# Optimization experiments

Measured on AMD Instinct MI355X. Metric: run time of the kernel, lower is better.

Reference implementation:

```python
import jax, jax.numpy as jnp
import numpy as np
from jax import lax

N = 16384      # total nodes (NG graphs x PER nodes)
PER = 512      # nodes per graph
NG = 32        # number of graphs
E = 262144     # edges (avg degree 16)
NEG = jnp.float32(-1e30)


def gcn_conv(x, W, b, src, dst, em, n):
    # PyG GCNConv: h = xW; add *remaining* self-loops; symmetric norm; aggregate at dst; + bias
    h = x @ W
    w = em.astype(x.dtype)
    selfw = jax.ops.segment_sum(jnp.where((src == dst) & em, 1.0, 0.0), dst, num_segments=n)
    has_self = (selfw > 0).astype(x.dtype)
    deg = jax.ops.segment_sum(w, dst, num_segments=n) + (1.0 - has_self)
    dinv = lax.rsqrt(deg)
    norm = dinv[src] * dinv[dst] * w                      # [E]
    agg = jax.ops.segment_sum(norm[:, None] * h[src], dst, num_segments=n)
    return agg + ((1.0 - has_self) / deg)[:, None] * h + b


def edge_pool(x, src, dst, em, nvalid, Pw, Pb, n):
    # PyG EdgePooling with softmax edge scores, add_to_edge_score=0.1, eval-mode dropout (identity)
    e = src.shape[0]
    raw = (jnp.concatenate([x[src], x[dst]], axis=1) @ Pw)[:, 0] + Pb[0]
    # softmax over edges grouped by target node
    logits = jnp.where(em, raw, NEG)
    mx = jax.ops.segment_max(logits, dst, num_segments=n)
    ex = jnp.where(em, jnp.exp(raw - mx[dst]), 0.0)
    den = jax.ops.segment_sum(ex, dst, num_segments=n)
    score = jnp.where(em, ex / jnp.maximum(den[dst], 1e-16), 0.0) + 0.1
    # greedy sequential edge contraction in descending score order (matches PyG __merge_edges__)
    key = lax.stop_gradient(jnp.where(em, score, NEG))
    order = jnp.argsort(-key)

    def step(marked, sdm):
        s, d, mk = sdm
        ok = mk & ~marked[s] & ~marked[d]
        m1 = marked.at[s].set(marked[s] | ok)
        m2 = m1.at[d].set(m1[d] | ok)
        return m2, ok

    _, ch_sorted = lax.scan(step, ~nvalid, (src[order], dst[order], em[order]))
    chosen = jnp.zeros(e, bool).at[order].set(ch_sorted)

    rep = jnp.minimum(src, dst)
    oth = jnp.maximum(src, dst)
    SEN = n  # out-of-range index -> dropped scatter
    cluster = jnp.arange(n, dtype=src.dtype).at[jnp.where(chosen, oth, SEN)].set(rep, mode='drop')
    node_score = jnp.ones(n, x.dtype).at[jnp.where(chosen, rep, SEN)].set(score, mode='drop')
    absorbed = jnp.zeros(n, bool).at[jnp.where(chosen & (src != dst), oth, SEN)].set(True, mode='drop')
    new_valid = nvalid & ~absorbed
    # new_x[c] = (sum of x over cluster) * edge score (1 for unmatched nodes)
    new_x = jax.ops.segment_sum(x, cluster, num_segments=n) * node_score[:, None]
    new_x = new_x * new_valid[:, None].astype(x.dtype)
    # remap + coalesce edges (dedupe); padding kept via mask
    ns, nd = cluster[src], cluster[dst]
    ekey = jnp.where(em, ns * n + nd, n * n)
    eo = jnp.argsort(ekey)
    ks = ekey[eo]
    dup = jnp.concatenate([jnp.zeros(1, bool), ks[1:] == ks[:-1]])
    return new_x, ns[eo], nd[eo], (ks < n * n) & ~dup, new_valid


def _forward(x, W1, b1, W2, b2, W3, b3, P1w, P1b, P2w, P2b, P3w, P3b,
             L1w, L1b, L2w, L2b, L3w, L3b, edge_index, batch):
    n = x.shape[0]
    src, dst = edge_index[0], edge_index[1]
    em = jnp.ones(src.shape[0], bool)
    nv = jnp.ones(n, bool)
    h = gcn_conv(x, W1, b1, src, dst, em, n)
    h, src, dst, em, nv = edge_pool(h, src, dst, em, nv, P1w, P1b, n)
    h = jax.nn.relu(h)
    h = gcn_conv(h, W2, b2, src, dst, em, n)
    h, src, dst, em, nv = edge_pool(h, src, dst, em, nv, P2w, P2b, n)
    h = jax.nn.relu(h)
    h = gcn_conv(h, W3, b3, src, dst, em, n)
    h, src, dst, em, nv = edge_pool(h, src, dst, em, nv, P3w, P3b, n)
    h = jax.nn.relu(h)
    beff = jnp.where(nv, batch, NG)                       # invalid nodes -> dummy segment
    g = jax.ops.segment_max(h, beff, num_segments=NG + 1)[:NG]
    z = jax.nn.relu(g @ L1w + L1b)
    z = jax.nn.relu(z @ L2w + L2b)
    z = jax.nn.relu(z @ L3w + L3b)
    return jax.nn.softmax(z, axis=-1)


def _lin(k, fi, fo):
    w = jax.random.normal(k, (fi, fo), jnp.float32) * (1.0 / np.sqrt(fi))
    return w, jnp.zeros((fo,), jnp.float32)


def setup_inputs() -> dict:
    key = jax.random.key(0)
    ks = jax.random.split(key, 16)
    x = jax.random.normal(ks[0], (N, 107), jnp.float32)
    src = jax.random.randint(ks[1], (E,), 0, N, dtype=jnp.int32)
    dst = (src // PER) * PER + jax.random.randint(ks[2], (E,), 0, PER, dtype=jnp.int32)
    edge_index = jnp.stack([src, dst])
    batch = jnp.arange(N, dtype=jnp.int32) // PER
    W1, b1 = _lin(ks[3], 107, 200)
    W2, b2 = _lin(ks[4], 200, 400)
    W3, b3 = _lin(ks[5], 400, 600)
    P1w, P1b = _lin(ks[6], 400, 1)
    P2w, P2b = _lin(ks[7], 800, 1)
    P3w, P3b = _lin(ks[8], 1200, 1)
    L1w, L1b = _lin(ks[9], 600, 200)
    L2w, L2b = _lin(ks[10], 200, 20)
    L3w, L3b = _lin(ks[11], 20, 4)
    return dict(x=x, edge_index=edge_index, batch=batch,
                W1=W1, b1=b1, W2=W2, b2=b2, W3=W3, b3=b3,
                P1w=P1w, P1b=P1b, P2w=P2w, P2b=P2b, P3w=P3w, P3b=P3b,
                L1w=L1w, L1b=L1b, L2w=L2w, L2b=L2b, L3w=L3w, L3b=L3b)


def reference(x, edge_index, batch, W1, b1, W2, b2, W3, b3,
              P1w, P1b, P2w, P2b, P3w, P3b, L1w, L1b, L2w, L2b, L3w, L3b):
    return _forward(x, W1, b1, W2, b2, W3, b3, P1w, P1b, P2w, P2b, P3w, P3b,
                    L1w, L1b, L2w, L2b, L3w, L3b, edge_index, batch)
```

## Files before the change

### kernel.cpp

```cpp
#include <hip/hip_runtime.h>

#define NN 16384
#define PERG 512
#define NGR 32
#define NE 262144
#define GSEG 9216

__device__ __forceinline__ unsigned encf(float f){
  unsigned u = __float_as_uint(f);
  return (u & 0x80000000u) ? ~u : (u | 0x80000000u);
}
__device__ __forceinline__ float decf(unsigned e){
  unsigned u = (e & 0x80000000u) ? (e ^ 0x80000000u) : ~e;
  return __uint_as_float(u);
}

__global__ void k_padx(const float* __restrict__ x, float* __restrict__ xp){
  int i = blockIdx.x*256 + threadIdx.x;
  if (i < NN*112){ int r = i/112, c = i-r*112; xp[i] = (c<107) ? x[r*107+c] : 0.f; }
}
__global__ void k_padw(const float* __restrict__ Wsrc, float* __restrict__ Wdst,
                       int Ksrc, int Kdst, int N){
  int i = blockIdx.x*256 + threadIdx.x;
  if (i < Kdst*N){ int r = i/N, c = i-r*N; Wdst[i] = (r<Ksrc) ? Wsrc[r*N+c] : 0.f; }
}

__global__ __launch_bounds__(256) void k_bucket(const int* __restrict__ ei, int* __restrict__ gcount,
    int* __restrict__ bsrc, int* __restrict__ bdst, int* __restrict__ bem, int* __restrict__ beid){
  __shared__ int cnt[NGR];
  __shared__ int base[NGR];
  int t = threadIdx.x;
  if (t < NGR) cnt[t] = 0;
  __syncthreads();
  int e = blockIdx.x*256 + t;
  int s=0,d=0,g=0,r=0;
  bool ok = (e < NE);
  if (ok){ s = ei[e]; d = ei[NE+e]; g = s >> 9; r = atomicAdd(&cnt[g],1); }
  __syncthreads();
  if (t < NGR) base[t] = atomicAdd(&gcount[t], cnt[t]);
  __syncthreads();
  if (ok){
    int pos = g*GSEG + base[g] + r;
    bsrc[pos]=s; bdst[pos]=d; bem[pos]=1; beid[pos]=e;
  }
}
__global__ void k_init_nodes(int* __restrict__ valid){
  int i = blockIdx.x*256 + threadIdx.x;
  if (i < NN) valid[i]=1;
}

__global__ __launch_bounds__(256) void k_mm(const float* __restrict__ A, const float* __restrict__ W,
                                            float* __restrict__ C, int KP, int N){
  __shared__ float As[16][132];
  __shared__ float Ws[16][132];
  int col0 = blockIdx.x*128, row0 = blockIdx.y*128;
  int t = threadIdx.x;
  int tx = t & 15, ty = t >> 4;
  int ar  = t >> 1;
  int akq0 = (t&1)*2, akq1 = (t&1)*2 + 1;
  int wk0 = (2*t) >> 5, wn0 = (2*t) & 31;
  int wk1 = (2*t+1) >> 5, wn1 = (2*t+1) & 31;
  int wc0 = col0 + wn0*4, wc1 = col0 + wn1*4;

  float4 a0,a1,w0,w1;
  auto loadT = [&](int k0){
    a0 = *(const float4*)&A[(size_t)(row0+ar)*KP + k0 + akq0*4];
    a1 = *(const float4*)&A[(size_t)(row0+ar)*KP + k0 + akq1*4];
    const float* p0 = &W[(size_t)(k0+wk0)*N + wc0];
    const float* p1 = &W[(size_t)(k0+wk1)*N + wc1];
    if (wc0+3 < N) w0 = *(const float4*)p0;
    else { w0.x=(wc0<N)?p0[0]:0.f; w0.y=(wc0+1<N)?p0[1]:0.f; w0.z=(wc0+2<N)?p0[2]:0.f; w0.w=0.f; }
    if (wc1+3 < N) w1 = *(const float4*)p1;
    else { w1.x=(wc1<N)?p1[0]:0.f; w1.y=(wc1+1<N)?p1[1]:0.f; w1.z=(wc1+2<N)?p1[2]:0.f; w1.w=0.f; }
  };
  auto storeT = [&](){
    As[akq0*4+0][ar]=a0.x; As[akq0*4+1][ar]=a0.y; As[akq0*4+2][ar]=a0.z; As[akq0*4+3][ar]=a0.w;
    As[akq1*4+0][ar]=a1.x; As[akq1*4+1][ar]=a1.y; As[akq1*4+2][ar]=a1.z; As[akq1*4+3][ar]=a1.w;
    *(float4*)&Ws[wk0][wn0*4] = w0;
    *(float4*)&Ws[wk1][wn1*4] = w1;
  };

  float acc[8][8];
#pragma unroll
  for (int i=0;i<8;i++)
#pragma unroll
    for (int j=0;j<8;j++) acc[i][j]=0.f;

  auto compute = [&](){
#pragma unroll
    for (int kk=0;kk<16;kk++){
      float4 A0 = *(const float4*)&As[kk][ty*4];
      float4 A1 = *(const float4*)&As[kk][64+ty*4];
      float4 B0 = *(const float4*)&Ws[kk][tx*4];
      float4 B1 = *(const float4*)&Ws[kk][64+tx*4];
      float a[8] = {A0.x,A0.y,A0.z,A0.w,A1.x,A1.y,A1.z,A1.w};
      float b[8] = {B0.x,B0.y,B0.z,B0.w,B1.x,B1.y,B1.z,B1.w};
#pragma unroll
      for (int i=0;i<8;i++)
#pragma unroll
        for (int j=0;j<8;j++) acc[i][j] += a[i]*b[j];
    }
  };

  loadT(0);
  storeT();
  __syncthreads();
  for (int k0=16; k0<KP; k0+=16){
    loadT(k0);
    compute();
    __syncthreads();
    storeT();
    __syncthreads();
  }
  compute();

#pragma unroll
  for (int i=0;i<8;i++){
    int r = row0 + ((i<4)? ty*4+i : 64+ty*4+(i-4));
#pragma unroll
    for (int j=0;j<8;j++){
      int cc = col0 + ((j<4)? tx*4+j : 64+tx*4+(j-4));
      if (cc<N) C[(size_t)r*N+cc] = acc[i][j];
    }
  }
}

__global__ __launch_bounds__(1024) void k_prep(const int* __restrict__ bsrc, const int* __restrict__ bdst,
    const int* __restrict__ bem, const int* __restrict__ gcount,
    int* __restrict__ row_s, int* __restrict__ row_e, int* __restrict__ elist,
    float* __restrict__ dinv, float* __restrict__ selfco){
  int g = blockIdx.x, t = threadIdx.x;
  __shared__ int cnt_l[PERG];
  __shared__ int scn[PERG];
  __shared__ int cur[PERG];
  __shared__ unsigned char hs_l[PERG];
  if (t<PERG){ cnt_l[t]=0; hs_l[t]=0; }
  __syncthreads();
  int nE = min(gcount[g], GSEG); int base = g*GSEG;
  for (int k=t;k<nE;k+=1024){
    if (bem[base+k]){
      int d = bdst[base+k]&511;
      atomicAdd(&cnt_l[d],1);
      if (bsrc[base+k]==bdst[base+k]) hs_l[d]=1;
    }
  }
  __syncthreads();
  if (t<PERG) scn[t]=cnt_l[t];
  __syncthreads();
  for (int off=1; off<PERG; off<<=1){
    int v = (t<PERG && t>=off) ? scn[t-off] : 0;
    __syncthreads();
    if (t<PERG) scn[t]+=v;
    __syncthreads();
  }
  if (t<PERG){
    int excl = scn[t]-cnt_l[t];
    row_s[g*PERG+t] = base+excl;
    row_e[g*PERG+t] = base+scn[t];
    cur[t] = excl;
    float deg = (float)cnt_l[t] + (hs_l[t]?0.f:1.f);
    dinv[g*PERG+t]   = rsqrtf(deg);
    selfco[g*PERG+t] = hs_l[t]?0.f:(1.f/deg);
  }
  __syncthreads();
  for (int k=t;k<nE;k+=1024){
    if (bem[base+k]){
      int d = bdst[base+k]&511;
      elist[base + atomicAdd(&cur[d],1)] = base+k;
    }
  }
}

template<int FO>
__global__ __launch_bounds__(256) void k_aggab(const float* __restrict__ h, const int* __restrict__ row_s,
    const int* __restrict__ row_e, const int* __restrict__ elist, const int* __restrict__ bsrc,
    const float* __restrict__ dinv, const float* __restrict__ selfco, const float* __restrict__ bias,
    const float* __restrict__ Pw, float* __restrict__ y, float* __restrict__ aval, float* __restrict__ bval){
  constexpr int Q = (FO+63)/64;
  int lane = threadIdx.x & 63;
  int nblk = (blockIdx.x & 7)*512 + (blockIdx.x >> 3);
  int i = nblk*4 + (threadIdx.x>>6);
  float acc[Q];
#pragma unroll
  for (int q=0;q<Q;q++) acc[q]=0.f;
  int s0 = row_s[i], s1 = row_e[i];
  float di = dinv[i];
  for (int p=s0; p<s1; p++){
    int e = elist[p]; int s = bsrc[e];
    float nr = di * dinv[s];
    const float* hrow = h + (size_t)s*FO;
#pragma unroll
    for (int q=0;q<Q;q++){ int c=lane+q*64; if (c<FO) acc[q] += nr*hrow[c]; }
  }
  float sc = selfco[i];
  const float* hi = h + (size_t)i*FO;
  float* yi = y + (size_t)i*FO;
  float sa=0.f, sb=0.f;
#pragma unroll
  for (int q=0;q<Q;q++){
    int c = lane+q*64;
    if (c<FO){
      float v = acc[q] + sc*hi[c] + bias[c];
      yi[c] = v;
      sa += v*Pw[c];
      sb += v*Pw[FO+c];
    }
  }
  for (int o=32;o;o>>=1){ sa += __shfl_xor(sa,o); sb += __shfl_xor(sb,o); }
  if (lane==0){ aval[i]=sa; bval[i]=sb; }
}

#define NEPT 9
__global__ __launch_bounds__(1024) void k_pool(const int* __restrict__ gcount,
    int* __restrict__ bsrc, int* __restrict__ bdst, int* __restrict__ bem, const int* __restrict__ beid,
    const float* __restrict__ aval, const float* __restrict__ bval, const float* __restrict__ Pb,
    float* __restrict__ nscore, int* __restrict__ partner, int* __restrict__ valid, int* __restrict__ table){
  int g = blockIdx.x, t = threadIdx.x;
  __shared__ unsigned mx[PERG];
  __shared__ float den[PERG];
  __shared__ unsigned long long best[PERG];
  __shared__ unsigned char marked[PERG];
  __shared__ unsigned short clus[PERG];
  __shared__ int flag;
  int nE = min(gcount[g], GSEG), base = g*GSEG;
  if (t<PERG){
    mx[t]=0u; den[t]=0.f;
    marked[t] = valid[g*PERG+t] ? 0 : 1;
    clus[t] = (unsigned short)t;
    nscore[g*PERG+t] = 1.f;
    partner[g*PERG+t] = -1;
  }
  __syncthreads();

  int sL[NEPT], dL[NEPT];
  float rawv[NEPT];
  unsigned em = 0u;
#pragma unroll
  for (int j=0;j<NEPT;j++){
    sL[j]=0; dL[j]=0; rawv[j]=0.f;
    int k = t + j*1024;
    if (k < nE && bem[base+k]){
      sL[j] = bsrc[base+k]&511; dL[j] = bdst[base+k]&511;
      rawv[j] = aval[(g<<9)+sL[j]] + bval[(g<<9)+dL[j]] + Pb[0];
      em |= (1u<<j);
      atomicMax(&mx[dL[j]], encf(rawv[j]));
    }
  }
  __syncthreads();
  float exv[NEPT];
#pragma unroll
  for (int j=0;j<NEPT;j++){
    exv[j]=0.f;
    if (em & (1u<<j)){
      exv[j] = expf(rawv[j] - decf(mx[dL[j]]));
      atomicAdd(&den[dL[j]], exv[j]);
    }
  }
  __syncthreads();
  unsigned long long pri[NEPT];
#pragma unroll
  for (int j=0;j<NEPT;j++){
    pri[j]=0ull;
    if (em & (1u<<j)){
      int k = t + j*1024;
      float sc = exv[j]/fmaxf(den[dL[j]],1e-16f) + 0.1f;
      pri[j] = ((unsigned long long)__float_as_uint(sc) << 18)
             | (unsigned long long)(0x3FFFFu - (unsigned)beid[base+k]);
    }
  }

  unsigned live = em;
  for (int round=0; round<512; ++round){
    if (t<PERG) best[t]=0ull;
    if (t==0) flag = 0;
    __syncthreads();
    int any = 0;
#pragma unroll
    for (int j=0;j<NEPT;j++){
      if (!(live & (1u<<j))) continue;
      int ls=sL[j], ld=dL[j];
      if (marked[ls] | marked[ld]){ live &= ~(1u<<j); continue; }
      any = 1;
      atomicMax(&best[ls], pri[j]);
      if (ld != ls) atomicMax(&best[ld], pri[j]);
    }
    if (any) flag = 1;
    __syncthreads();
    if (!flag) break;
#pragma unroll
    for (int j=0;j<NEPT;j++){
      if (!(live & (1u<<j))) continue;
      int ls=sL[j], ld=dL[j];
      unsigned long long p = pri[j];
      if (best[ls]==p && best[ld]==p){
        int repl = min(ls,ld), oth = max(ls,ld);
        clus[oth] = (unsigned short)repl;
        nscore[g*PERG+repl] = __uint_as_float((unsigned)(p>>18));
        if (ls != ld){ valid[g*PERG+oth] = 0; partner[g*PERG+repl] = g*PERG+oth; }
        marked[ls] = 1; marked[ld] = 1;
        live &= ~(1u<<j);
      }
    }
    __syncthreads();
  }
  __syncthreads();

#pragma unroll
  for (int j=0;j<NEPT;j++){
    if (em & (1u<<j)){
      int k = t + j*1024;
      int ns = clus[sL[j]], nd = clus[dL[j]];
      sL[j]=ns; dL[j]=nd;
      bsrc[base+k] = (g<<9)+ns; bdst[base+k] = (g<<9)+nd;
      table[(g<<18) | (ns<<9) | nd] = 0x7FFFFFFF;
    }
  }
  __syncthreads();
#pragma unroll
  for (int j=0;j<NEPT;j++){
    if (em & (1u<<j)){
      int k = t + j*1024;
      atomicMin(&table[(g<<18) | (sL[j]<<9) | dL[j]], base+k);
    }
  }
  __syncthreads();
#pragma unroll
  for (int j=0;j<NEPT;j++){
    if (em & (1u<<j)){
      int k = t + j*1024;
      if (table[(g<<18) | (sL[j]<<9) | dL[j]] != base+k) bem[base+k] = 0;
    }
  }
}

template<int FO, int FOP>
__global__ __launch_bounds__(256) void k_newx(const float* __restrict__ y, const int* __restrict__ partner,
    const float* __restrict__ nscore, const int* __restrict__ valid, float* __restrict__ out){
  constexpr int Q = (FOP+63)/64;
  int lane = threadIdx.x & 63;
  int nblk = (blockIdx.x & 7)*512 + (blockIdx.x >> 3);
  int i = nblk*4 + (threadIdx.x>>6);
  int v = valid[i];
  float ns = nscore[i];
  int p = partner[i];
  const float* yi = y + (size_t)i*FO;
  const float* yp = (p>=0) ? (y + (size_t)p*FO) : yi;
  float* oi = out + (size_t)i*FOP;
#pragma unroll
  for (int q=0;q<Q;q++){
    int c = lane + q*64;
    if (c<FO){
      float val = yi[c];
      if (p>=0) val += yp[c];
      val *= ns;
      oi[c] = v ? fmaxf(val,0.f) : 0.f;
    } else if (c<FOP){
      oi[c] = 0.f;
    }
  }
}

__global__ __launch_bounds__(256) void k_gmax(const float* __restrict__ x, const int* __restrict__ valid,
                                              float* __restrict__ gbuf){
  int g = blockIdx.x;
  __shared__ int lv[PERG];
  for (int i=threadIdx.x;i<PERG;i+=256) lv[i] = valid[g*PERG+i];
  __syncthreads();
  const float* base = x + (size_t)g*PERG*600;
  for (int c=threadIdx.x; c<600; c+=256){
    float m = -1e30f;
    for (int r=0;r<PERG;r++)
      if (lv[r]) m = fmaxf(m, base[(size_t)r*600+c]);
    gbuf[g*600+c] = m;
  }
}
__global__ __launch_bounds__(256) void k_head(const float* __restrict__ gbuf,
    const float* __restrict__ L1w, const float* __restrict__ L1b,
    const float* __restrict__ L2w, const float* __restrict__ L2b,
    const float* __restrict__ L3w, const float* __restrict__ L3b, float* __restrict__ out){
  int g = blockIdx.x, t = threadIdx.x;
  __shared__ float gg[600];
  __shared__ float z1[200];
  __shared__ float z2[20];
  __shared__ float z3[4];
  for (int c=t;c<600;c+=256) gg[c] = gbuf[g*600+c];
  __syncthreads();
  if (t<200){
    float s = L1b[t];
    for (int k=0;k<600;k++) s += gg[k]*L1w[k*200+t];
    z1[t] = fmaxf(s,0.f);
  }
  __syncthreads();
  if (t<20){
    float s = L2b[t];
    for (int k=0;k<200;k++) s += z1[k]*L2w[k*20+t];
    z2[t] = fmaxf(s,0.f);
  }
  __syncthreads();
  if (t<4){
    float s = L3b[t];
    for (int k=0;k<20;k++) s += z2[k]*L3w[k*4+t];
    z3[t] = fmaxf(s,0.f);
  }
  __syncthreads();
  if (t==0){
    float m = fmaxf(fmaxf(z3[0],z3[1]), fmaxf(z3[2],z3[3]));
    float e0=expf(z3[0]-m), e1=expf(z3[1]-m), e2=expf(z3[2]-m), e3=expf(z3[3]-m);
    float s = e0+e1+e2+e3;
    out[g*4+0]=e0/s; out[g*4+1]=e1/s; out[g*4+2]=e2/s; out[g*4+3]=e3/s;
  }
}

struct WsPtrs {
  float *A, *B, *x0p, *W1p, *W2p;
  int *bsrc, *bdst, *bem, *beid;
  int *elist, *row_s, *row_e;
  float *dinv, *selfco, *aval, *bval;
  float *nscore; int *partner; int *valid;
  int *gcount;
  float *gbuf;
};

extern "C" void kernel_launch(void* const* d_in, const int* in_sizes, int n_in,
                              void* d_out, int out_size, void* d_ws, size_t ws_size,
                              hipStream_t stream){
  const float* x0  = (const float*)d_in[0];
  const int*   ei  = (const int*)  d_in[1];
  const float* W1  = (const float*)d_in[3];  const float* b1  = (const float*)d_in[4];
  const float* W2  = (const float*)d_in[5];  const float* b2  = (const float*)d_in[6];
  const float* W3  = (const float*)d_in[7];  const float* b3  = (const float*)d_in[8];
  const float* P1w = (const float*)d_in[9];  const float* P1b = (const float*)d_in[10];
  const float* P2w = (const float*)d_in[11]; const float* P2b = (const float*)d_in[12];
  const float* P3w = (const float*)d_in[13]; const float* P3b = (const float*)d_in[14];
  const float* L1w = (const float*)d_in[15]; const float* L1b = (const float*)d_in[16];
  const float* L2w = (const float*)d_in[17]; const float* L2b = (const float*)d_in[18];
  const float* L3w = (const float*)d_in[19]; const float* L3b = (const float*)d_in[20];
  float* out = (float*)d_out;

  char* w = (char*)d_ws;
  size_t off = 0;
  auto alloc = [&](size_t bytes)->void*{
    void* p = w + off;
    off += bytes;
    off = (off + 255) & ~(size_t)255;
    return p;
  };
  WsPtrs P;
  P.A     = (float*)alloc((size_t)NN*600*4);
  P.B     = (float*)alloc((size_t)NN*600*4);
  P.x0p   = (float*)alloc((size_t)NN*112*4);
  P.W1p   = (float*)alloc((size_t)112*200*4);
  P.W2p   = (float*)alloc((size_t)208*400*4);
  P.bsrc  = (int*)  alloc((size_t)NGR*GSEG*4);
  P.bdst  = (int*)  alloc((size_t)NGR*GSEG*4);
  P.bem   = (int*)  alloc((size_t)NGR*GSEG*4);
  P.beid  = (int*)  alloc((size_t)NGR*GSEG*4);
  P.elist = (int*)  alloc((size_t)NGR*GSEG*4);
  P.row_s = (int*)  alloc((size_t)NN*4);
  P.row_e = (int*)  alloc((size_t)NN*4);
  P.dinv   = (float*)alloc((size_t)NN*4);
  P.selfco = (float*)alloc((size_t)NN*4);
  P.aval   = (float*)alloc((size_t)NN*4);
  P.bval   = (float*)alloc((size_t)NN*4);
  P.nscore = (float*)alloc((size_t)NN*4);
  P.partner= (int*)  alloc((size_t)NN*4);
  P.valid  = (int*)  alloc((size_t)NN*4);
  P.gcount = (int*)  alloc((size_t)NGR*4);
  P.gbuf   = (float*)alloc((size_t)NGR*600*4);
  (void)ws_size; (void)in_sizes; (void)n_in; (void)out_size;

  const int NG4 = NN/4;

  k_padx<<<(NN*112+255)/256,256,0,stream>>>(x0, P.x0p);
  k_padw<<<(112*200+255)/256,256,0,stream>>>(W1, P.W1p, 107, 112, 200);
  k_padw<<<(208*400+255)/256,256,0,stream>>>(W2, P.W2p, 200, 208, 400);
  hipMemsetAsync(P.gcount, 0, NGR*sizeof(int), stream);
  k_bucket<<<NE/256,256,0,stream>>>(ei, P.gcount, P.bsrc, P.bdst, P.bem, P.beid);
  k_init_nodes<<<NN/256,256,0,stream>>>(P.valid);

  { dim3 gmm(2,128); k_mm<<<gmm,256,0,stream>>>(P.x0p, P.W1p, P.A, 112, 200); }
  k_prep<<<NGR,1024,0,stream>>>(P.bsrc,P.bdst,P.bem,P.gcount,P.row_s,P.row_e,P.elist,P.dinv,P.selfco);
  k_aggab<200><<<NG4,256,0,stream>>>(P.A,P.row_s,P.row_e,P.elist,P.bsrc,P.dinv,P.selfco,b1,P1w,P.B,P.aval,P.bval);
  k_pool<<<NGR,1024,0,stream>>>(P.gcount,P.bsrc,P.bdst,P.bem,P.beid,P.aval,P.bval,P1b,
                                P.nscore,P.partner,P.valid,(int*)P.A);
  k_newx<200,208><<<NG4,256,0,stream>>>(P.B,P.partner,P.nscore,P.valid,P.A);

  { dim3 gmm(4,128); k_mm<<<gmm,256,0,stream>>>(P.A, P.W2p, P.B, 208, 400); }
  k_prep<<<NGR,1024,0,stream>>>(P.bsrc,P.bdst,P.bem,P.gcount,P.row_s,P.row_e,P.elist,P.dinv,P.selfco);
  k_aggab<400><<<NG4,256,0,stream>>>(P.B,P.row_s,P.row_e,P.elist,P.bsrc,P.dinv,P.selfco,b2,P2w,P.A,P.aval,P.bval);
  k_pool<<<NGR,1024,0,stream>>>(P.gcount,P.bsrc,P.bdst,P.bem,P.beid,P.aval,P.bval,P2b,
                                P.nscore,P.partner,P.valid,(int*)P.B);
  k_newx<400,400><<<NG4,256,0,stream>>>(P.A,P.partner,P.nscore,P.valid,P.B);

  { dim3 gmm(5,128); k_mm<<<gmm,256,0,stream>>>(P.B, W3, P.A, 400, 600); }
  k_prep<<<NGR,1024,0,stream>>>(P.bsrc,P.bdst,P.bem,P.gcount,P.row_s,P.row_e,P.elist,P.dinv,P.selfco);
  k_aggab<600><<<NG4,256,0,stream>>>(P.A,P.row_s,P.row_e,P.elist,P.bsrc,P.dinv,P.selfco,b3,P3w,P.B,P.aval,P.bval);
  k_pool<<<NGR,1024,0,stream>>>(P.gcount,P.bsrc,P.bdst,P.bem,P.beid,P.aval,P.bval,P3b,
                                P.nscore,P.partner,P.valid,(int*)P.A);
  k_newx<600,600><<<NG4,256,0,stream>>>(P.B,P.partner,P.nscore,P.valid,P.A);

  k_gmax<<<NGR,256,0,stream>>>(P.A, P.valid, P.gbuf);
  k_head<<<NGR,256,0,stream>>>(P.gbuf, L1w, L1b, L2w, L2b, L3w, L3b, out);
}
```

Measured before the change: 1.144 ms.

## Shrink GEMM column tile to 64 and split graph max-pool across blocks

Result: faster. 988.2 us (-13.6%).

```diff
diff --git a/kernel.cpp b/kernel.cpp
--- a/kernel.cpp
+++ b/kernel.cpp
@@ -52,75 +52,60 @@
 __global__ __launch_bounds__(256) void k_mm(const float* __restrict__ A, const float* __restrict__ W,
                                             float* __restrict__ C, int KP, int N){
   __shared__ float As[16][132];
-  __shared__ float Ws[16][132];
-  int col0 = blockIdx.x*128, row0 = blockIdx.y*128;
+  __shared__ float Ws[16][68];
+  int col0 = blockIdx.x*64, row0 = blockIdx.y*128;
   int t = threadIdx.x;
   int tx = t & 15, ty = t >> 4;
-  int ar  = t >> 1;
-  int akq0 = (t&1)*2, akq1 = (t&1)*2 + 1;
-  int wk0 = (2*t) >> 5, wn0 = (2*t) & 31;
-  int wk1 = (2*t+1) >> 5, wn1 = (2*t+1) & 31;
-  int wc0 = col0 + wn0*4, wc1 = col0 + wn1*4;
-
-  float4 a0,a1,w0,w1;
-  auto loadT = [&](int k0){
-    a0 = *(const float4*)&A[(size_t)(row0+ar)*KP + k0 + akq0*4];
-    a1 = *(const float4*)&A[(size_t)(row0+ar)*KP + k0 + akq1*4];
-    const float* p0 = &W[(size_t)(k0+wk0)*N + wc0];
-    const float* p1 = &W[(size_t)(k0+wk1)*N + wc1];
-    if (wc0+3 < N) w0 = *(const float4*)p0;
-    else { w0.x=(wc0<N)?p0[0]:0.f; w0.y=(wc0+1<N)?p0[1]:0.f; w0.z=(wc0+2<N)?p0[2]:0.f; w0.w=0.f; }
-    if (wc1+3 < N) w1 = *(const float4*)p1;
-    else { w1.x=(wc1<N)?p1[0]:0.f; w1.y=(wc1+1<N)?p1[1]:0.f; w1.z=(wc1+2<N)?p1[2]:0.f; w1.w=0.f; }
-  };
-  auto storeT = [&](){
-    As[akq0*4+0][ar]=a0.x; As[akq0*4+1][ar]=a0.y; As[akq0*4+2][ar]=a0.z; As[akq0*4+3][ar]=a0.w;
-    As[akq1*4+0][ar]=a1.x; As[akq1*4+1][ar]=a1.y; As[akq1*4+2][ar]=a1.z; As[akq1*4+3][ar]=a1.w;
-    *(float4*)&Ws[wk0][wn0*4] = w0;
-    *(float4*)&Ws[wk1][wn1*4] = w1;
-  };
-
-  float acc[8][8];
+  int ar = t >> 1;
+  int ak = (t & 1) * 8;
+  int wk = t >> 4;
+  int wn = (t & 15) * 4;
+  int wc = col0 + wn;
+
+  float acc[8][4];
 #pragma unroll
   for (int i=0;i<8;i++)
 #pragma unroll
-    for (int j=0;j<8;j++) acc[i][j]=0.f;
-
-  auto compute = [&](){
+    for (int j=0;j<4;j++) acc[i][j]=0.f;
+
+  const float* Arow = A + (size_t)(row0+ar)*KP;
+
+  for (int k0=0; k0<KP; k0+=16){
+    float4 a0 = *(const float4*)&Arow[k0 + ak];
+    float4 a1 = *(const float4*)&Arow[k0 + ak + 4];
+    float4 w0;
+    const float* wp = &W[(size_t)(k0+wk)*N + wc];
+    if (wc+3 < N) w0 = *(const float4*)wp;
+    else { w0.x=(wc<N)?wp[0]:0.f; w0.y=(wc+1<N)?wp[1]:0.f; w0.z=(wc+2<N)?wp[2]:0.f; w0.w=0.f; }
+    __syncthreads();
+    As[ak+0][ar]=a0.x; As[ak+1][ar]=a0.y; As[ak+2][ar]=a0.z; As[ak+3][ar]=a0.w;
+    As[ak+4][ar]=a1.x; As[ak+5][ar]=a1.y; As[ak+6][ar]=a1.z; As[ak+7][ar]=a1.w;
+    *(float4*)&Ws[wk][wn] = w0;
+    __syncthreads();
 #pragma unroll
     for (int kk=0;kk<16;kk++){
-      float4 A0 = *(const float4*)&As[kk][ty*4];
-      float4 A1 = *(const float4*)&As[kk][64+ty*4];
+      float4 A0 = *(const float4*)&As[kk][ty*8];
+      float4 A1 = *(const float4*)&As[kk][ty*8+4];
       float4 B0 = *(const float4*)&Ws[kk][tx*4];
-      float4 B1 = *(const float4*)&Ws[kk][64+tx*4];
       float a[8] = {A0.x,A0.y,A0.z,A0.w,A1.x,A1.y,A1.z,A1.w};
-      float b[8] = {B0.x,B0.y,B0.z,B0.w,B1.x,B1.y,B1.z,B1.w};
+      float b[4] = {B0.x,B0.y,B0.z,B0.w};
 #pragma unroll
       for (int i=0;i<8;i++)
 #pragma unroll
-        for (int j=0;j<8;j++) acc[i][j] += a[i]*b[j];
-    }
-  };
-
-  loadT(0);
-  storeT();
-  __syncthreads();
-  for (int k0=16; k0<KP; k0+=16){
-    loadT(k0);
-    compute();
-    __syncthreads();
-    storeT();
-    __syncthreads();
-  }
-  compute();
+        for (int j=0;j<4;j++) acc[i][j] += a[i]*b[j];
+    }
+  }
 
 #pragma unroll
   for (int i=0;i<8;i++){
-    int r = row0 + ((i<4)? ty*4+i : 64+ty*4+(i-4));
-#pragma unroll
-    for (int j=0;j<8;j++){
-      int cc = col0 + ((j<4)? tx*4+j : 64+tx*4+(j-4));
-      if (cc<N) C[(size_t)r*N+cc] = acc[i][j];
+    int r = row0 + ty*8 + i;
+    int cc = col0 + tx*4;
+    if (cc+3 < N){
+      float4 v = {acc[i][0],acc[i][1],acc[i][2],acc[i][3]};
+      *(float4*)&C[(size_t)r*N+cc] = v;
+    } else {
+#pragma unroll
+      for (int j=0;j<4;j++) if (cc+j<N) C[(size_t)r*N+cc+j] = acc[i][j];
     }
   }
 }
@@ -361,20 +346,21 @@
 }
 
 __global__ __launch_bounds__(256) void k_gmax(const float* __restrict__ x, const int* __restrict__ valid,
-                                              float* __restrict__ gbuf){
-  int g = blockIdx.x;
-  __shared__ int lv[PERG];
-  for (int i=threadIdx.x;i<PERG;i+=256) lv[i] = valid[g*PERG+i];
-  __syncthreads();
-  const float* base = x + (size_t)g*PERG*600;
+                                              float* __restrict__ part){
+  int g = blockIdx.x >> 3, rp = blockIdx.x & 7;
+  __shared__ int lv[64];
+  int r0 = rp*64;
+  if (threadIdx.x < 64) lv[threadIdx.x] = valid[g*PERG + r0 + threadIdx.x];
+  __syncthreads();
+  const float* base = x + ((size_t)g*PERG + r0)*600;
   for (int c=threadIdx.x; c<600; c+=256){
     float m = -1e30f;
-    for (int r=0;r<PERG;r++)
+    for (int r=0;r<64;r++)
       if (lv[r]) m = fmaxf(m, base[(size_t)r*600+c]);
-    gbuf[g*600+c] = m;
-  }
-}
-__global__ __launch_bounds__(256) void k_head(const float* __restrict__ gbuf,
+    part[(size_t)(g*8+rp)*600 + c] = m;
+  }
+}
+__global__ __launch_bounds__(256) void k_head(const float* __restrict__ part,
     const float* __restrict__ L1w, const float* __restrict__ L1b,
     const float* __restrict__ L2w, const float* __restrict__ L2b,
     const float* __restrict__ L3w, const float* __restrict__ L3b, float* __restrict__ out){
@@ -383,16 +369,23 @@
   __shared__ float z1[200];
   __shared__ float z2[20];
   __shared__ float z3[4];
-  for (int c=t;c<600;c+=256) gg[c] = gbuf[g*600+c];
+  for (int c=t;c<600;c+=256){
+    float m = -1e30f;
+#pragma unroll
+    for (int rp=0;rp<8;rp++) m = fmaxf(m, part[(size_t)(g*8+rp)*600 + c]);
+    gg[c] = m;
+  }
   __syncthreads();
   if (t<200){
     float s = L1b[t];
+#pragma unroll 4
     for (int k=0;k<600;k++) s += gg[k]*L1w[k*200+t];
     z1[t] = fmaxf(s,0.f);
   }
   __syncthreads();
   if (t<20){
     float s = L2b[t];
+#pragma unroll 4
     for (int k=0;k<200;k++) s += z1[k]*L2w[k*20+t];
     z2[t] = fmaxf(s,0.f);
   }
@@ -466,7 +459,7 @@
   P.partner= (int*)  alloc((size_t)NN*4);
   P.valid  = (int*)  alloc((size_t)NN*4);
   P.gcount = (int*)  alloc((size_t)NGR*4);
-  P.gbuf   = (float*)alloc((size_t)NGR*600*4);
+  P.gbuf   = (float*)alloc((size_t)NGR*8*600*4);
   (void)ws_size; (void)in_sizes; (void)n_in; (void)out_size;
 
   const int NG4 = NN/4;
@@ -478,27 +471,27 @@
   k_bucket<<<NE/256,256,0,stream>>>(ei, P.gcount, P.bsrc, P.bdst, P.bem, P.beid);
   k_init_nodes<<<NN/256,256,0,stream>>>(P.valid);
 
-  { dim3 gmm(2,128); k_mm<<<gmm,256,0,stream>>>(P.x0p, P.W1p, P.A, 112, 200); }
+  { dim3 gmm(4,128); k_mm<<<gmm,256,0,stream>>>(P.x0p, P.W1p, P.A, 112, 200); }
   k_prep<<<NGR,1024,0,stream>>>(P.bsrc,P.bdst,P.bem,P.gcount,P.row_s,P.row_e,P.elist,P.dinv,P.selfco);
   k_aggab<200><<<NG4,256,0,stream>>>(P.A,P.row_s,P.row_e,P.elist,P.bsrc,P.dinv,P.selfco,b1,P1w,P.B,P.aval,P.bval);
   k_pool<<<NGR,1024,0,stream>>>(P.gcount,P.bsrc,P.bdst,P.bem,P.beid,P.aval,P.bval,P1b,
                                 P.nscore,P.partner,P.valid,(int*)P.A);
   k_newx<200,208><<<NG4,256,0,stream>>>(P.B,P.partner,P.nscore,P.valid,P.A);
 
-  { dim3 gmm(4,128); k_mm<<<gmm,256,0,stream>>>(P.A, P.W2p, P.B, 208, 400); }
+  { dim3 gmm(7,128); k_mm<<<gmm,256,0,stream>>>(P.A, P.W2p, P.B, 208, 400); }
   k_prep<<<NGR,1024,0,stream>>>(P.bsrc,P.bdst,P.bem,P.gcount,P.row_s,P.row_e,P.elist,P.dinv,P.selfco);
   k_aggab<400><<<NG4,256,0,stream>>>(P.B,P.row_s,P.row_e,P.elist,P.bsrc,P.dinv,P.selfco,b2,P2w,P.A,P.aval,P.bval);
   k_pool<<<NGR,1024,0,stream>>>(P.gcount,P.bsrc,P.bdst,P.bem,P.beid,P.aval,P.bval,P2b,
                                 P.nscore,P.partner,P.valid,(int*)P.B);
   k_newx<400,400><<<NG4,256,0,stream>>>(P.A,P.partner,P.nscore,P.valid,P.B);
 
-  { dim3 gmm(5,128); k_mm<<<gmm,256,0,stream>>>(P.B, W3, P.A, 400, 600); }
+  { dim3 gmm(10,128); k_mm<<<gmm,256,0,stream>>>(P.B, W3, P.A, 400, 600); }
   k_prep<<<NGR,1024,0,stream>>>(P.bsrc,P.bdst,P.bem,P.gcount,P.row_s,P.row_e,P.elist,P.dinv,P.selfco);
   k_aggab<600><<<NG4,256,0,stream>>>(P.A,P.row_s,P.row_e,P.elist,P.bsrc,P.dinv,P.selfco,b3,P3w,P.B,P.aval,P.bval);
   k_pool<<<NGR,1024,0,stream>>>(P.gcount,P.bsrc,P.bdst,P.bem,P.beid,P.aval,P.bval,P3b,
                                 P.nscore,P.partner,P.valid,(int*)P.A);
   k_newx<600,600><<<NG4,256,0,stream>>>(P.B,P.partner,P.nscore,P.valid,P.A);
 
-  k_gmax<<<NGR,256,0,stream>>>(P.A, P.valid, P.gbuf);
+  k_gmax<<<NGR*8,256,0,stream>>>(P.A, P.valid, P.gbuf);
   k_head<<<NGR,256,0,stream>>>(P.gbuf, L1w, L1b, L2w, L2b, L3w, L3b, out);
 }
```
